# Optimization experiments

Hardware: AMD Instinct MI355X
Metric: run time of the kernel (lower is better)

The kernel has to match this reference:

```python
import jax, jax.numpy as jnp
import numpy as np
from jax import lax

VOL = (128, 192, 192)
PATCH = (64, 64, 64)
DOWN = (4, 4, 4)
C = 8
STRIDE = 32


def gaussian_importance_map(patch_size, sigma_scale=0.125):
    # MONAI-style separable gaussian centered at size//2, sigma = size*sigma_scale,
    # normalized to max 1, zero values clamped to smallest positive value.
    axes = []
    for s in patch_size:
        center = s // 2
        sigma = sigma_scale * s
        x = jnp.arange(s, dtype=jnp.float32)
        axes.append(jnp.exp(-0.5 * ((x - center) / sigma) ** 2))
    w = axes[0][:, None, None] * axes[1][None, :, None] * axes[2][None, None, :]
    w = w / w.max()
    pos_min = jnp.min(jnp.where(w > 0, w, jnp.inf))
    return jnp.maximum(w, pos_min)  # [Hp, Wp, Dp]


def make_grid_starts():
    zs = np.arange(0, VOL[0] - PATCH[0] + 1, STRIDE)
    ys = np.arange(0, VOL[1] - PATCH[1] + 1, STRIDE)
    xs = np.arange(0, VOL[2] - PATCH[2] + 1, STRIDE)
    g = np.stack(np.meshgrid(zs, ys, xs, indexing='ij'), axis=-1).reshape(-1, 3)
    return jnp.asarray(g, dtype=jnp.int32)  # [75, 3]


def setup_inputs() -> dict:
    key = jax.random.key(0)
    k1, k2 = jax.random.split(key)
    starts = make_grid_starts()
    n = starts.shape[0]
    logit_patches = jax.random.normal(k1, (n, C) + PATCH, dtype=jnp.float32)
    hg, wg, dg = (VOL[0] // DOWN[0], VOL[1] // DOWN[1], VOL[2] // DOWN[2])
    global_logit = jax.random.normal(k2, (1, C, hg, wg, dg), dtype=jnp.float32)
    return {"logit_patches": logit_patches, "global_logit": global_logit, "starts": starts}


def reference(logit_patches, global_logit, starts):
    wt = gaussian_importance_map(PATCH)[None, None]  # [1,1,Hp,Wp,Dp]

    # trilinear upsample (align_corners=False semantics, half-pixel centers)
    up_global = jax.image.resize(global_logit, (1, C) + VOL, method='trilinear')

    final_logit = jnp.zeros((1, C) + VOL, dtype=jnp.float32)
    weight_map = jnp.full((1, 1) + VOL, 1e-20, dtype=jnp.float32)
    mask = jnp.zeros((1, 1) + VOL, dtype=jnp.float32)
    ones_patch = jnp.ones((1, 1) + PATCH, dtype=jnp.float32)

    def body(carry, inp):
        fl, wm, mk = carry
        patch, st = inp
        idx5 = (0, 0, st[0], st[1], st[2])
        cur = lax.dynamic_slice(fl, idx5, (1, C) + PATCH)
        fl = lax.dynamic_update_slice(fl, cur + patch[None] * wt, idx5)
        curw = lax.dynamic_slice(wm, idx5, (1, 1) + PATCH)
        wm = lax.dynamic_update_slice(wm, curw + wt, idx5)
        mk = lax.dynamic_update_slice(mk, ones_patch, idx5)
        return (fl, wm, mk), None

    (final_logit, weight_map, mask), _ = lax.scan(
        body, (final_logit, weight_map, mask), (logit_patches, starts))

    final_logit = final_logit / weight_map
    final_logit = final_logit + jnp.where(mask == 1.0, 0.0, up_global)
    return final_logit
```

## Files before the change

kernel.cpp:

```cpp
#include <hip/hip_runtime.h>

#define VZ 128
#define VY 192
#define VX 192
#define NC 8
#define PS 64

struct F4 { float x, y, z, w; };

__global__ __launch_bounds__(192)
void agg_kernel(const float* __restrict__ patches, float* __restrict__ out)
{
    __shared__ float g[PS];
    const int t = threadIdx.y * 48 + threadIdx.x;
    if (t < PS) {
        const float d = ((float)t - 32.0f) * 0.125f;
        g[t] = __expf(-0.5f * d * d);
    }
    __syncthreads();

    const int x0 = threadIdx.x << 2;
    const int y  = blockIdx.x * 4 + threadIdx.y;
    const int z  = blockIdx.y;
    const int c  = blockIdx.z;

    const int szh = min(64,  (z  >> 5) << 5);
    const int szl = szh - 32;
    const bool z2 = (szl >= 0) && ((z - szl) < PS);
    const int syh = min(128, (y  >> 5) << 5);
    const int syl = syh - 32;
    const bool y2 = (syl >= 0) && ((y - syl) < PS);
    const int sxh = min(128, (x0 >> 5) << 5);
    const int sxl = sxh - 32;
    const bool x2 = (sxl >= 0) && ((x0 - sxl) < PS);

    const F4* g4 = (const F4*)g;
    const F4 wxh = g4[(x0 - sxh) >> 2];
    F4 wxl = {0.f, 0.f, 0.f, 0.f};
    if (x2) wxl = g4[(x0 - sxl) >> 2];
    const float gzh = g[z - szh];
    const float gyh = g[y - syh];
    const float gzl = z2 ? g[z - szl] : 0.0f;
    const float gyl = y2 ? g[y - syl] : 0.0f;

    float a0 = 0.f, a1 = 0.f, a2 = 0.f, a3 = 0.f;
    float w0 = 1e-20f, w1 = 1e-20f, w2 = 1e-20f, w3 = 1e-20f;

#define PROC(SZ, SY, SX, WZY, WX)                                             \
    do {                                                                      \
        const int p = (((SZ) >> 5) * 5 + ((SY) >> 5)) * 5 + ((SX) >> 5);      \
        const size_t off = ((((size_t)(p * NC + c) * PS + (size_t)(z - (SZ))) \
                             * PS + (size_t)(y - (SY)))                       \
                            * PS + (size_t)(x0 - (SX)));                      \
        const F4 pv = *(const F4*)(patches + off);                            \
        const float wzy = (WZY);                                              \
        a0 += pv.x * (wzy * (WX).x);  w0 += wzy * (WX).x;                     \
        a1 += pv.y * (wzy * (WX).y);  w1 += wzy * (WX).y;                     \
        a2 += pv.z * (wzy * (WX).z);  w2 += wzy * (WX).z;                     \
        a3 += pv.w * (wzy * (WX).w);  w3 += wzy * (WX).w;                     \
    } while (0)

    PROC(szh, syh, sxh, gzh * gyh, wxh);
    if (x2) PROC(szh, syh, sxl, gzh * gyh, wxl);
    if (y2) {
        PROC(szh, syl, sxh, gzh * gyl, wxh);
        if (x2) PROC(szh, syl, sxl, gzh * gyl, wxl);
    }
    if (z2) {
        PROC(szl, syh, sxh, gzl * gyh, wxh);
        if (x2) PROC(szl, syh, sxl, gzl * gyh, wxl);
        if (y2) {
            PROC(szl, syl, sxh, gzl * gyl, wxh);
            if (x2) PROC(szl, syl, sxl, gzl * gyl, wxl);
        }
    }
#undef PROC

    F4 r;
    r.x = a0 / w0;
    r.y = a1 / w1;
    r.z = a2 / w2;
    r.w = a3 / w3;
    const size_t oidx = (((size_t)c * VZ + z) * VY + y) * VX + x0;
    *(F4*)(out + oidx) = r;
}

extern "C" void kernel_launch(void* const* d_in, const int* in_sizes, int n_in,
                              void* d_out, int out_size, void* d_ws, size_t ws_size,
                              hipStream_t stream) {
    const float* patches = (const float*)d_in[0];
    float* out = (float*)d_out;

    dim3 block(48, 4, 1);
    dim3 grid(VY / 4, VZ, NC);
    agg_kernel<<<grid, block, 0, stream>>>(patches, out);
}
```

Before: 157.5 us.

## Tile blocks to 32x32 patch-aligned regions, process two channels per thread

Reshapes blocks into 8x32 threads covering a 32x32 xy tile aligned to the patch stride, so overlap flags become block-uniform and branches do not diverge. Each thread now handles two channels, reusing the weight sums and reciprocal across both. Loads and stores become nontemporal vector ops, and division becomes a fast hardware reciprocal. Risks include slightly lower precision from rcp and fewer blocks in the grid.

```diff
diff --git a/kernel.cpp b/kernel.cpp
--- a/kernel.cpp
+++ b/kernel.cpp
@@ -5,59 +5,64 @@
 #define VX 192
 #define NC 8
 #define PS 64
+#define PS3 (PS * PS * PS)
 
-struct F4 { float x, y, z, w; };
+typedef float f4 __attribute__((ext_vector_type(4)));
 
-__global__ __launch_bounds__(192)
+__global__ __launch_bounds__(256)
 void agg_kernel(const float* __restrict__ patches, float* __restrict__ out)
 {
     __shared__ float g[PS];
-    const int t = threadIdx.y * 48 + threadIdx.x;
+    const int t = threadIdx.y * 8 + threadIdx.x;
     if (t < PS) {
         const float d = ((float)t - 32.0f) * 0.125f;
         g[t] = __expf(-0.5f * d * d);
     }
     __syncthreads();
 
-    const int x0 = threadIdx.x << 2;
-    const int y  = blockIdx.x * 4 + threadIdx.y;
+    const int bx = blockIdx.x % 6;
+    const int by = blockIdx.x / 6;
+    const int x0 = bx * 32 + (threadIdx.x << 2);
+    const int y  = by * 32 + threadIdx.y;
     const int z  = blockIdx.y;
-    const int c  = blockIdx.z;
+    const int c0 = blockIdx.z << 1;
 
-    const int szh = min(64,  (z  >> 5) << 5);
+    const int szh = min(64, (z >> 5) << 5);
     const int szl = szh - 32;
-    const bool z2 = (szl >= 0) && ((z - szl) < PS);
-    const int syh = min(128, (y  >> 5) << 5);
+    const bool z2 = (z >= 32) & (z < 96);
+    const int syh = min(128, by * 32);
     const int syl = syh - 32;
-    const bool y2 = (syl >= 0) && ((y - syl) < PS);
-    const int sxh = min(128, (x0 >> 5) << 5);
+    const bool y2 = (by >= 1) & (by <= 4);
+    const int sxh = min(128, bx * 32);
     const int sxl = sxh - 32;
-    const bool x2 = (sxl >= 0) && ((x0 - sxl) < PS);
+    const bool x2 = (bx >= 1) & (bx <= 4);
 
-    const F4* g4 = (const F4*)g;
-    const F4 wxh = g4[(x0 - sxh) >> 2];
-    F4 wxl = {0.f, 0.f, 0.f, 0.f};
+    const f4* g4 = (const f4*)g;
+    const f4 wxh = g4[(x0 - sxh) >> 2];
+    f4 wxl = {0.f, 0.f, 0.f, 0.f};
     if (x2) wxl = g4[(x0 - sxl) >> 2];
     const float gzh = g[z - szh];
     const float gyh = g[y - syh];
     const float gzl = z2 ? g[z - szl] : 0.0f;
     const float gyl = y2 ? g[y - syl] : 0.0f;
 
-    float a0 = 0.f, a1 = 0.f, a2 = 0.f, a3 = 0.f;
-    float w0 = 1e-20f, w1 = 1e-20f, w2 = 1e-20f, w3 = 1e-20f;
+    f4 acc0 = {0.f, 0.f, 0.f, 0.f};
+    f4 acc1 = {0.f, 0.f, 0.f, 0.f};
+    f4 wsum = {1e-20f, 1e-20f, 1e-20f, 1e-20f};
 
-#define PROC(SZ, SY, SX, WZY, WX)                                             \
-    do {                                                                      \
-        const int p = (((SZ) >> 5) * 5 + ((SY) >> 5)) * 5 + ((SX) >> 5);      \
-        const size_t off = ((((size_t)(p * NC + c) * PS + (size_t)(z - (SZ))) \
-                             * PS + (size_t)(y - (SY)))                       \
-                            * PS + (size_t)(x0 - (SX)));                      \
-        const F4 pv = *(const F4*)(patches + off);                            \
-        const float wzy = (WZY);                                              \
-        a0 += pv.x * (wzy * (WX).x);  w0 += wzy * (WX).x;                     \
-        a1 += pv.y * (wzy * (WX).y);  w1 += wzy * (WX).y;                     \
-        a2 += pv.z * (wzy * (WX).z);  w2 += wzy * (WX).z;                     \
-        a3 += pv.w * (wzy * (WX).w);  w3 += wzy * (WX).w;                     \
+#define PROC(SZ, SY, SX, WZY, WX)                                              \
+    do {                                                                       \
+        const int p = (((SZ) >> 5) * 5 + ((SY) >> 5)) * 5 + ((SX) >> 5);       \
+        const size_t base = ((size_t)(p * NC + c0)) * PS3 +                    \
+            (((size_t)(z - (SZ)) * PS + (size_t)(y - (SY))) * PS) +            \
+            (size_t)(x0 - (SX));                                               \
+        const f4 cw = (WZY) * (WX);                                            \
+        wsum += cw;                                                            \
+        const f4 pv0 = __builtin_nontemporal_load((const f4*)(patches + base));\
+        const f4 pv1 = __builtin_nontemporal_load(                             \
+            (const f4*)(patches + base + PS3));                                \
+        acc0 += pv0 * cw;                                                      \
+        acc1 += pv1 * cw;                                                      \
     } while (0)
 
     PROC(szh, syh, sxh, gzh * gyh, wxh);
@@ -76,13 +81,16 @@
     }
 #undef PROC
 
-    F4 r;
-    r.x = a0 / w0;
-    r.y = a1 / w1;
-    r.z = a2 / w2;
-    r.w = a3 / w3;
-    const size_t oidx = (((size_t)c * VZ + z) * VY + y) * VX + x0;
-    *(F4*)(out + oidx) = r;
+    f4 inv;
+    inv.x = __builtin_amdgcn_rcpf(wsum.x);
+    inv.y = __builtin_amdgcn_rcpf(wsum.y);
+    inv.z = __builtin_amdgcn_rcpf(wsum.z);
+    inv.w = __builtin_amdgcn_rcpf(wsum.w);
+
+    const size_t ob = (((size_t)c0 * VZ + z) * VY + y) * VX + x0;
+    __builtin_nontemporal_store(acc0 * inv, (f4*)(out + ob));
+    __builtin_nontemporal_store(acc1 * inv,
+                                (f4*)(out + ob + (size_t)VZ * VY * VX));
 }
 
 extern "C" void kernel_launch(void* const* d_in, const int* in_sizes, int n_in,
@@ -91,7 +99,7 @@
     const float* patches = (const float*)d_in[0];
     float* out = (float*)d_out;
 
-    dim3 block(48, 4, 1);
-    dim3 grid(VY / 4, VZ, NC);
+    dim3 block(8, 32, 1);
+    dim3 grid(6 * 6, VZ, NC / 2);
     agg_kernel<<<grid, block, 0, stream>>>(patches, out);
 }
```

New measurement: 148.8 us. 1.06x faster.
